# Optimization experiments

Measured on AMD Instinct MI355X. Metric: run time of the kernel, lower is better.

The kernel has to match this reference:

```python
import jax, jax.numpy as jnp
import numpy as np

N = 50000      # nodes
E = 800000     # edges
F = 64         # in_channels == out_channels
ED = 16        # edge_dim
G = 64         # graphs in batch
L = 2          # numLayers
BN_EPS = 1e-5
STD_EPS = 1e-5
AGG_DIM = F * 4 * 3  # 4 aggregators x 3 scalers


def setup_inputs() -> dict:
    key = jax.random.key(0)
    ks = jax.random.split(key, 12)
    r = lambda k, shp, fan: (jax.random.normal(k, shp, jnp.float32) / np.sqrt(fan)).astype(jnp.float32)
    return dict(
        x=jax.random.normal(ks[0], (N, F), jnp.float32),
        edge_attr=jax.random.normal(ks[1], (E, ED), jnp.float32),
        We=r(ks[2], (L, ED, F), ED), be=jnp.zeros((L, F), jnp.float32),
        Wpre=r(ks[3], (L, 3 * F, F), 3 * F), bpre=jnp.zeros((L, F), jnp.float32),
        Wpost=r(ks[4], (L, F + AGG_DIM, F), F + AGG_DIM), bpost=jnp.zeros((L, F), jnp.float32),
        Wlin=r(ks[5], (L, F, F), F), blin=jnp.zeros((L, F), jnp.float32),
        gamma=jnp.ones((L, F), jnp.float32), beta=jnp.zeros((L, F), jnp.float32),
        W1=r(ks[6], (F, 40), F), b1=jnp.zeros((40,), jnp.float32),
        W2=r(ks[7], (40, 1), 40), b2=jnp.zeros((1,), jnp.float32),
        edge_index=jax.random.randint(ks[8], (2, E), 0, N),
        batch=jnp.sort(jax.random.randint(ks[9], (N,), 0, G)),
    )


def _ceal_conv(x, src, dst, edge_attr, We, be, Wpre, bpre, Wpost, bpost, Wlin, blin, deg, amp, att):
    # PNA-style conv, towers=1, pre_layers=post_layers=1
    e = edge_attr @ We + be                                              # [E,F]
    h = jnp.concatenate([x[dst], x[src], e], axis=-1) @ Wpre + bpre      # [E,F]
    degc = jnp.maximum(deg, 1.0)[:, None]
    mean = jax.ops.segment_sum(h, dst, num_segments=N) / degc
    sq = jax.ops.segment_sum(h * h, dst, num_segments=N) / degc
    std = jnp.sqrt(jax.nn.relu(sq - mean * mean) + STD_EPS)
    has = (deg > 0)[:, None]
    mn = jnp.where(has, jax.ops.segment_min(h, dst, num_segments=N), 0.0)
    mx = jnp.where(has, jax.ops.segment_max(h, dst, num_segments=N), 0.0)
    aggs = jnp.concatenate([mean, mn, mx, std], axis=-1)                 # [N,4F]
    scaled = jnp.concatenate([aggs, aggs * amp[:, None], aggs * att[:, None]], axis=-1)  # [N,12F]
    out = jnp.concatenate([x, scaled], axis=-1) @ Wpost + bpost          # [N,F]
    return out @ Wlin + blin


def _bn(x, gamma, beta):
    mu = x.mean(0)
    var = x.var(0)  # biased, as torch BatchNorm training-mode normalization
    return (x - mu) * jax.lax.rsqrt(var + BN_EPS) * gamma + beta


def reference(x, edge_attr, We, be, Wpre, bpre, Wpost, bpost, Wlin, blin,
              gamma, beta, W1, b1, W2, b2, edge_index, batch):
    src, dst = edge_index[0], edge_index[1]
    deg = jax.ops.segment_sum(jnp.ones((E,), jnp.float32), dst, num_segments=N)
    avg_log = jnp.mean(jnp.log(deg + 1.0))
    logd = jnp.log(jnp.maximum(deg, 1.0) + 1.0)
    amp = logd / avg_log
    att = avg_log / logd
    for l in range(L):
        x = _ceal_conv(x, src, dst, edge_attr, We[l], be[l], Wpre[l], bpre[l],
                       Wpost[l], bpost[l], Wlin[l], blin[l], deg, amp, att)
        x = jax.nn.relu(_bn(x, gamma[l], beta[l]))
    cnt = jnp.maximum(jax.ops.segment_sum(jnp.ones((N,), jnp.float32), batch, num_segments=G), 1.0)
    gm = jax.ops.segment_sum(x, batch, num_segments=G) / cnt[:, None]    # global_mean_pool [G,F]
    return jax.nn.relu(gm @ W1 + b1) @ W2 + b2                           # [G,1]
```

## Files before the change

### kernel.cpp

```cpp
#include <hip/hip_runtime.h>
#include <math.h>
#include <float.h>

#define NN 50000
#define EE 800000
#define FF 64
#define EDIM 16
#define GG 64
#define NB64 782
#define NSB 196

typedef short bf16x8 __attribute__((ext_vector_type(8)));
typedef float f32x4 __attribute__((ext_vector_type(4)));

__device__ inline unsigned short bf_rne(float v) {
  unsigned int u = __float_as_uint(v);
  unsigned int r = (u + 0x7FFFu + ((u >> 16) & 1u)) >> 16;
  return (unsigned short)r;
}
__device__ inline float bf_up(unsigned short h) {
  return __uint_as_float(((unsigned int)h) << 16);
}
__device__ inline void split4(float4 v, ushort4& h, ushort4& l) {
  h.x = bf_rne(v.x); h.y = bf_rne(v.y); h.z = bf_rne(v.z); h.w = bf_rne(v.w);
  l.x = bf_rne(v.x - bf_up(h.x));
  l.y = bf_rne(v.y - bf_up(h.y));
  l.z = bf_rne(v.z - bf_up(h.z));
  l.w = bf_rne(v.w - bf_up(h.w));
}

__global__ __launch_bounds__(256) void k_zfill(int* __restrict__ deg, int* __restrict__ cursor,
                                               int* __restrict__ srcs_slack, float* __restrict__ psum) {
  int i = blockIdx.x * 256 + threadIdx.x;
  if (i < NN) { deg[i] = 0; cursor[i] = 0; }
  if (i < 16) srcs_slack[i] = 0;
  if (i < GG * FF + GG) psum[i] = 0.0f;
}

__global__ void k_deg(const int* __restrict__ eidx, int* __restrict__ deg) {
  int e = blockIdx.x * 256 + threadIdx.x;
  if (e < EE) atomicAdd(&deg[eidx[EE + e]], 1);
}

__global__ __launch_bounds__(256) void k_scanA(const int* __restrict__ deg, int* __restrict__ offsets,
                                               int* __restrict__ bsum, float* __restrict__ lsum) {
  __shared__ int ws[4];
  __shared__ float lw[4];
  int t = threadIdx.x;
  int lane = t & 63;
  int wv = t >> 6;
  int i = blockIdx.x * 256 + t;
  int v = (i < NN) ? deg[i] : 0;
  float lg = (i < NN) ? logf((float)v + 1.0f) : 0.0f;
  int x = v;
  #pragma unroll
  for (int o = 1; o < 64; o <<= 1) {
    int y = __shfl_up(x, o);
    if (lane >= o) x += y;
  }
  #pragma unroll
  for (int o = 1; o < 64; o <<= 1) lg += __shfl_xor(lg, o);
  if (lane == 63) ws[wv] = x;
  if (lane == 0) lw[wv] = lg;
  __syncthreads();
  int pre = 0;
  for (int k = 0; k < wv; k++) pre += ws[k];
  if (i < NN) offsets[i] = pre + x - v;
  if (t == 0) {
    bsum[blockIdx.x] = ws[0] + ws[1] + ws[2] + ws[3];
    lsum[blockIdx.x] = lw[0] + lw[1] + lw[2] + lw[3];
  }
}

__global__ __launch_bounds__(256) void k_scanB(const int* __restrict__ bsum, const float* __restrict__ lsum,
                                               int* __restrict__ bpref, float* __restrict__ meta,
                                               float* __restrict__ scbA) {
  __shared__ int ws[4];
  __shared__ float lw[4];
  int t = threadIdx.x;
  int lane = t & 63;
  int wv = t >> 6;
  int v = (t < NSB) ? bsum[t] : 0;
  float lg = (t < NSB) ? lsum[t] : 0.0f;
  int x = v;
  #pragma unroll
  for (int o = 1; o < 64; o <<= 1) {
    int y = __shfl_up(x, o);
    if (lane >= o) x += y;
  }
  #pragma unroll
  for (int o = 1; o < 64; o <<= 1) lg += __shfl_xor(lg, o);
  if (lane == 63) ws[wv] = x;
  if (lane == 0) lw[wv] = lg;
  __syncthreads();
  int pre = 0;
  for (int k = 0; k < wv; k++) pre += ws[k];
  if (t < NSB) bpref[t] = pre + x - v;
  if (t == 0) meta[0] = (lw[0] + lw[1] + lw[2] + lw[3]) / (float)NN;
  if (t < 64) { scbA[t] = 1.0f; scbA[64 + t] = 0.0f; }
  if (t == 0) scbA[128] = -FLT_MAX;
}

__global__ __launch_bounds__(256) void k_scanC(int* __restrict__ offsets, const int* __restrict__ bpref,
                                               const int* __restrict__ deg, const float* __restrict__ meta,
                                               float* __restrict__ amp, float* __restrict__ att) {
  int i = blockIdx.x * 256 + threadIdx.x;
  if (i < NN) {
    offsets[i] += bpref[blockIdx.x];
    float d = (float)deg[i];
    float avg = meta[0];
    float logd = logf(fmaxf(d, 1.0f) + 1.0f);
    amp[i] = logd / avg;
    att[i] = avg / logd;
  }
  if (i == 0) offsets[NN] = EE;
}

__global__ void k_scatter(const int* __restrict__ eidx, const int* __restrict__ offsets,
                          int* __restrict__ cursor, int* __restrict__ srcs,
                          const float* __restrict__ eattr, unsigned int* __restrict__ PermEA) {
  int e = blockIdx.x * 256 + threadIdx.x;
  if (e < EE) {
    int s = eidx[e];
    int d = eidx[EE + e];
    int pos = offsets[d] + atomicAdd(&cursor[d], 1);
    srcs[pos] = s;
    const float4* ep = (const float4*)(eattr + (size_t)e * EDIM);
    float4 q0 = ep[0], q1 = ep[1], q2 = ep[2], q3 = ep[3];
    uint4 pa, pb;
    pa.x = (unsigned)bf_rne(q0.x) | ((unsigned)bf_rne(q0.y) << 16);
    pa.y = (unsigned)bf_rne(q0.z) | ((unsigned)bf_rne(q0.w) << 16);
    pa.z = (unsigned)bf_rne(q1.x) | ((unsigned)bf_rne(q1.y) << 16);
    pa.w = (unsigned)bf_rne(q1.z) | ((unsigned)bf_rne(q1.w) << 16);
    pb.x = (unsigned)bf_rne(q2.x) | ((unsigned)bf_rne(q2.y) << 16);
    pb.y = (unsigned)bf_rne(q2.z) | ((unsigned)bf_rne(q2.w) << 16);
    pb.z = (unsigned)bf_rne(q3.x) | ((unsigned)bf_rne(q3.y) << 16);
    pb.w = (unsigned)bf_rne(q3.z) | ((unsigned)bf_rne(q3.w) << 16);
    ((uint4*)PermEA)[(size_t)pos * 2] = pa;
    ((uint4*)PermEA)[(size_t)pos * 2 + 1] = pb;
  }
}

__global__ __launch_bounds__(256) void k_prep2(const float* __restrict__ We, const float* __restrict__ be,
                                               const float* __restrict__ Wpre, const float* __restrict__ bpre,
                                               const float* __restrict__ Wpost, const float* __restrict__ bpost,
                                               const float* __restrict__ Wlin, const float* __restrict__ blin,
                                               unsigned short* __restrict__ MwT_h, unsigned short* __restrict__ MwT_l,
                                               float* __restrict__ bconst,
                                               unsigned short* __restrict__ WcT_h, unsigned short* __restrict__ WcT_l,
                                               unsigned short* __restrict__ WxT_h, unsigned short* __restrict__ WxT_l,
                                               float* __restrict__ bcomb) {
  int layer = blockIdx.x / 245;
  int blk = blockIdx.x % 245;
  We += (size_t)layer * EDIM * FF;  be += layer * FF;
  Wpre += (size_t)layer * 3 * FF * FF; bpre += layer * FF;
  Wpost += (size_t)layer * 832 * FF; bpost += layer * FF;
  Wlin += (size_t)layer * FF * FF; blin += layer * FF;
  MwT_h += layer * 1024; MwT_l += layer * 1024;
  bconst += layer * FF; bcomb += layer * FF;
  WcT_h += (size_t)layer * 53248; WcT_l += (size_t)layer * 53248;
  WxT_h += layer * 8192; WxT_l += layer * 8192;

  int id = blk * 256 + threadIdx.x;
  if (id < 53248) {
    int k = id >> 6, f = id & 63;
    float a = 0.0f;
    for (int j = 0; j < FF; j++) a += Wpost[(size_t)k * FF + j] * Wlin[j * FF + f];
    unsigned short h = bf_rne(a);
    WcT_h[f * 832 + k] = h;
    WcT_l[f * 832 + k] = bf_rne(a - bf_up(h));
  } else if (id < 61440) {
    int lid = id - 53248;
    int j = lid >> 6, k = lid & 63;
    float v = (j < 64) ? Wpre[k * FF + j] : Wpre[(64 + k) * FF + (j - 64)];
    unsigned short h = bf_rne(v);
    WxT_h[j * 64 + k] = h;
    WxT_l[j * 64 + k] = bf_rne(v - bf_up(h));
  } else if (id < 62464) {
    int lid = id - 61440;
    int k = lid >> 6, f = lid & 63;
    float a = 0.0f;
    for (int j = 0; j < FF; j++) a += We[k * FF + j] * Wpre[(128 + j) * FF + f];
    unsigned short h = bf_rne(a);
    int ct = f & 3, jcol = f >> 2;
    MwT_h[(ct * 16 + jcol) * 16 + k] = h;
    MwT_l[(ct * 16 + jcol) * 16 + k] = bf_rne(a - bf_up(h));
  } else {
    int f = threadIdx.x;
    if (blk == 244 && f < 64) {
      float b = bpre[f];
      for (int j = 0; j < FF; j++) b += be[j] * Wpre[(128 + j) * FF + f];
      bconst[f] = b;
      float c = blin[f];
      for (int j = 0; j < FF; j++) c += bpost[j] * Wlin[j * FF + f];
      bcomb[f] = c;
    }
  }
}

__global__ __launch_bounds__(256) void k_xform(const float* __restrict__ x, const float* __restrict__ scb,
                                               const unsigned short* __restrict__ WxT_h,
                                               const unsigned short* __restrict__ WxT_l,
                                               float* __restrict__ Xd, unsigned short* __restrict__ Xs) {
  __shared__ unsigned short Ah[64 * 72], Al[64 * 72];
  __shared__ unsigned short Bh[128 * 72], Bl[128 * 72];
  int t = threadIdx.x;
  int n0 = blockIdx.x * 64;
  {
    int j = t >> 1, half = t & 1;
    const ushort4* srch = (const ushort4*)(WxT_h + j * 64 + half * 32);
    const ushort4* srcl = (const ushort4*)(WxT_l + j * 64 + half * 32);
    #pragma unroll
    for (int i = 0; i < 8; i++) {
      *(ushort4*)&Bh[j * 72 + half * 32 + i * 4] = srch[i];
      *(ushort4*)&Bl[j * 72 + half * 32 + i * 4] = srcl[i];
    }
  }
  {
    int r = t >> 2, c0 = (t & 3) * 16;
    int n = n0 + r;
    bool rok = n < NN;
    const float4* src = (const float4*)(x + (size_t)n * FF + c0);
    float flr = scb[128];
    #pragma unroll
    for (int c4 = 0; c4 < 4; c4++) {
      float4 v = rok ? src[c4] : make_float4(0.f, 0.f, 0.f, 0.f);
      float4 sc = ((const float4*)scb)[(c0 >> 2) + c4];
      float4 of = ((const float4*)(scb + 64))[(c0 >> 2) + c4];
      v.x = fmaxf(v.x * sc.x + of.x, flr);
      v.y = fmaxf(v.y * sc.y + of.y, flr);
      v.z = fmaxf(v.z * sc.z + of.z, flr);
      v.w = fmaxf(v.w * sc.w + of.w, flr);
      ushort4 h4, l4;
      split4(v, h4, l4);
      *(ushort4*)&Ah[r * 72 + c0 + c4 * 4] = h4;
      *(ushort4*)&Al[r * 72 + c0 + c4 * 4] = l4;
    }
  }
  __syncthreads();
  int lane = t & 63;
  int l15 = lane & 15;
  int quad = lane >> 4;
  int w = __builtin_amdgcn_readfirstlane(t >> 6);
  int rbase = (w & 1) * 32;
  int cbase = (w >> 1) * 64;
  f32x4 acc[2][4];
  #pragma unroll
  for (int rt = 0; rt < 2; rt++)
    #pragma unroll
    for (int ct = 0; ct < 4; ct++) acc[rt][ct] = (f32x4){0.f, 0.f, 0.f, 0.f};

  #pragma unroll
  for (int ks = 0; ks < 2; ks++) {
    bf16x8 a_h[2], a_l[2];
    #pragma unroll
    for (int rt = 0; rt < 2; rt++) {
      int row = rbase + rt * 16 + l15;
      a_h[rt] = *(const bf16x8*)&Ah[row * 72 + ks * 32 + quad * 8];
      a_l[rt] = *(const bf16x8*)&Al[row * 72 + ks * 32 + quad * 8];
    }
    #pragma unroll
    for (int ct = 0; ct < 4; ct++) {
      int col = cbase + ct * 16 + l15;
      bf16x8 b_h = *(const bf16x8*)&Bh[col * 72 + ks * 32 + quad * 8];
      bf16x8 b_l = *(const bf16x8*)&Bl[col * 72 + ks * 32 + quad * 8];
      #pragma unroll
      for (int rt = 0; rt < 2; rt++) {
        acc[rt][ct] = __builtin_amdgcn_mfma_f32_16x16x32_bf16(a_h[rt], b_h, acc[rt][ct], 0, 0, 0);
        acc[rt][ct] = __builtin_amdgcn_mfma_f32_16x16x32_bf16(a_h[rt], b_l, acc[rt][ct], 0, 0, 0);
        acc[rt][ct] = __builtin_amdgcn_mfma_f32_16x16x32_bf16(a_l[rt], b_h, acc[rt][ct], 0, 0, 0);
      }
    }
  }
  #pragma unroll
  for (int rt = 0; rt < 2; rt++) {
    #pragma unroll
    for (int ct = 0; ct < 4; ct++) {
      int col = cbase + ct * 16 + l15;
      #pragma unroll
      for (int reg = 0; reg < 4; reg++) {
        int n = n0 + rbase + rt * 16 + quad * 4 + reg;
        if (n < NN) {
          float v = acc[rt][ct][reg];
          if (col < 64) Xd[(size_t)n * FF + col] = v;
          else          Xs[(size_t)n * FF + (col - 64)] = bf_rne(v);
        }
      }
    }
  }
}

__global__ __launch_bounds__(256) void k_agg(const int* __restrict__ srcs, const int* __restrict__ offsets,
                                             const unsigned int* __restrict__ PermEA,
                                             const unsigned short* __restrict__ MwT_h,
                                             const unsigned short* __restrict__ MwT_l,
                                             const float* __restrict__ bconst,
                                             const float* __restrict__ Xd, const unsigned short* __restrict__ Xs,
                                             unsigned short* __restrict__ aggs) {
  int wid = __builtin_amdgcn_readfirstlane(threadIdx.x >> 6);
  int lane = threadIdx.x & 63;
  int l15 = lane & 15;
  int quad = lane >> 4;
  int n = blockIdx.x * 4 + wid;
  if (n >= NN) return;

  bf16x8 bh[4], bl[4];
  #pragma unroll
  for (int ct = 0; ct < 4; ct++) {
    if (quad < 2) {
      bh[ct] = *(const bf16x8*)&MwT_h[(ct * 16 + l15) * 16 + quad * 8];
      bl[ct] = *(const bf16x8*)&MwT_l[(ct * 16 + l15) * 16 + quad * 8];
    } else {
      bh[ct] = (bf16x8){0, 0, 0, 0, 0, 0, 0, 0};
      bl[ct] = (bf16x8){0, 0, 0, 0, 0, 0, 0, 0};
    }
  }

  float4 xd4 = *(const float4*)(Xd + (size_t)n * FF + 4 * l15);
  float4 bc4 = *(const float4*)(bconst + 4 * l15);
  float bas[4] = {xd4.x + bc4.x, xd4.y + bc4.y, xd4.z + bc4.z, xd4.w + bc4.w};

  int o0 = offsets[n], o1 = offsets[n + 1];
  float s[4]  = {0.f, 0.f, 0.f, 0.f};
  float sq[4] = {0.f, 0.f, 0.f, 0.f};
  float mn[4] = {FLT_MAX, FLT_MAX, FLT_MAX, FLT_MAX};
  float mx[4] = {-FLT_MAX, -FLT_MAX, -FLT_MAX, -FLT_MAX};

  for (int base = o0; base < o1; base += 16) {
    bf16x8 af = (bf16x8){0, 0, 0, 0, 0, 0, 0, 0};
    if (quad < 2) af = *(const bf16x8*)(PermEA + (size_t)(base + l15) * 8 + quad * 4);
    f32x4 acc[4];
    #pragma unroll
    for (int ct = 0; ct < 4; ct++) {
      f32x4 a = (f32x4){0.f, 0.f, 0.f, 0.f};
      a = __builtin_amdgcn_mfma_f32_16x16x32_bf16(af, bl[ct], a, 0, 0, 0);
      a = __builtin_amdgcn_mfma_f32_16x16x32_bf16(af, bh[ct], a, 0, 0, 0);
      acc[ct] = a;
    }
    #pragma unroll
    for (int reg = 0; reg < 4; reg++) {
      int e = base + quad * 4 + reg;
      bool valid = e < o1;
      int ec = min(e, o1 - 1);
      int src = srcs[ec];
      ushort4 xs4 = *(const ushort4*)(Xs + (size_t)src * FF + 4 * l15);
      float xf[4] = {bf_up(xs4.x), bf_up(xs4.y), bf_up(xs4.z), bf_up(xs4.w)};
      #pragma unroll
      for (int ct = 0; ct < 4; ct++) {
        float h = bas[ct] + xf[ct] + acc[ct][reg];
        float hv = valid ? h : 0.0f;
        s[ct] += hv;
        sq[ct] = fmaf(hv, hv, sq[ct]);
        float t1 = fminf(mn[ct], h);
        float t2 = fmaxf(mx[ct], h);
        mn[ct] = valid ? t1 : mn[ct];
        mx[ct] = valid ? t2 : mx[ct];
      }
    }
  }

  #pragma unroll
  for (int ct = 0; ct < 4; ct++) {
    s[ct] += __shfl_xor(s[ct], 16);  s[ct] += __shfl_xor(s[ct], 32);
    sq[ct] += __shfl_xor(sq[ct], 16); sq[ct] += __shfl_xor(sq[ct], 32);
    mn[ct] = fminf(mn[ct], __shfl_xor(mn[ct], 16)); mn[ct] = fminf(mn[ct], __shfl_xor(mn[ct], 32));
    mx[ct] = fmaxf(mx[ct], __shfl_xor(mx[ct], 16)); mx[ct] = fmaxf(mx[ct], __shfl_xor(mx[ct], 32));
  }

  float d = (float)(o1 - o0);
  float dc = fmaxf(d, 1.0f);
  float rdc = 1.0f / dc;
  bool has = d > 0.0f;
  ushort4 outv;
  unsigned short ov[4];
  #pragma unroll
  for (int ct = 0; ct < 4; ct++) {
    float mean = s[ct] * rdc;
    float msq = sq[ct] * rdc;
    float sd = sqrtf(fmaxf(msq - mean * mean, 0.0f) + 1e-5f);
    float vmn = has ? mn[ct] : 0.0f;
    float vmx = has ? mx[ct] : 0.0f;
    float val = (quad == 0) ? mean : (quad == 1) ? vmn : (quad == 2) ? vmx : sd;
    ov[ct] = bf_rne(val);
  }
  outv.x = ov[0]; outv.y = ov[1]; outv.z = ov[2]; outv.w = ov[3];
  *(ushort4*)(aggs + (size_t)n * 256 + quad * 64 + 4 * l15) = outv;
}

__global__ __launch_bounds__(256) void k_post(const float* __restrict__ x, const float* __restrict__ scb,
                                              const unsigned short* __restrict__ aggs,
                                              const float* __restrict__ amp, const float* __restrict__ att,
                                              const unsigned short* __restrict__ WcT_h,
                                              const unsigned short* __restrict__ WcT_l,
                                              const float* __restrict__ bcomb,
                                              float* __restrict__ y, float* __restrict__ partials) {
  __shared__ unsigned short Ah[64 * 72], Al[64 * 72];
  __shared__ unsigned short Bh[64 * 72], Bl[64 * 72];
  __shared__ float red_s[4][32], red_q[4][32];
  int t = threadIdx.x;
  int n0 = blockIdx.x * 64;
  int lane = t & 63;
  int l15 = lane & 15;
  int quad = lane >> 4;
  int w = __builtin_amdgcn_readfirstlane(t >> 6);
  int rbase = (w & 1) * 32;
  int cbase = (w >> 1) * 32;

  int ar = t >> 2;
  int ac0 = (t & 3) * 16;
  int an = n0 + ar;
  bool rok = an < NN;
  const float* xrow = x + (size_t)an * FF;
  const unsigned short* arow = aggs + (size_t)an * 256;
  float flr = scb[128];

  f32x4 acc[3][2][2];
  #pragma unroll
  for (int s = 0; s < 3; s++)
    #pragma unroll
    for (int rt = 0; rt < 2; rt++)
      #pragma unroll
      for (int ct = 0; ct < 2; ct++) acc[s][rt][ct] = (f32x4){0.f, 0.f, 0.f, 0.f};

  {
    #pragma unroll
    for (int c4 = 0; c4 < 4; c4++) {
      float4 v = rok ? *(const float4*)(xrow + ac0 + c4 * 4) : make_float4(0.f, 0.f, 0.f, 0.f);
      float4 sc = ((const float4*)scb)[(ac0 >> 2) + c4];
      float4 of = ((const float4*)(scb + 64))[(ac0 >> 2) + c4];
      v.x = fmaxf(v.x * sc.x + of.x, flr);
      v.y = fmaxf(v.y * sc.y + of.y, flr);
      v.z = fmaxf(v.z * sc.z + of.z, flr);
      v.w = fmaxf(v.w * sc.w + of.w, flr);
      ushort4 h4, l4;
      split4(v, h4, l4);
      *(ushort4*)&Ah[ar * 72 + ac0 + c4 * 4] = h4;
      *(ushort4*)&Al[ar * 72 + ac0 + c4 * 4] = l4;
    }
    const ushort4* sh = (const ushort4*)(WcT_h + ar * 832 + ac0);
    const ushort4* sl = (const ushort4*)(WcT_l + ar * 832 + ac0);
    #pragma unroll
    for (int i = 0; i < 4; i++) {
      *(ushort4*)&Bh[ar * 72 + ac0 + i * 4] = sh[i];
      *(ushort4*)&Bl[ar * 72 + ac0 + i * 4] = sl[i];
    }
    __syncthreads();
    #pragma unroll
    for (int ks = 0; ks < 2; ks++) {
      bf16x8 a_h[2], a_l[2], b_h[2], b_l[2];
      #pragma unroll
      for (int rt = 0; rt < 2; rt++) {
        int row = rbase + rt * 16 + l15;
        a_h[rt] = *(const bf16x8*)&Ah[row * 72 + ks * 32 + quad * 8];
        a_l[rt] = *(const bf16x8*)&Al[row * 72 + ks * 32 + quad * 8];
      }
      #pragma unroll
      for (int ct = 0; ct < 2; ct++) {
        int col = cbase + ct * 16 + l15;
        b_h[ct] = *(const bf16x8*)&Bh[col * 72 + ks * 32 + quad * 8];
        b_l[ct] = *(const bf16x8*)&Bl[col * 72 + ks * 32 + quad * 8];
      }
      #pragma unroll
      for (int rt = 0; rt < 2; rt++)
        #pragma unroll
        for (int ct = 0; ct < 2; ct++) {
          acc[0][rt][ct] = __builtin_amdgcn_mfma_f32_16x16x32_bf16(a_h[rt], b_h[ct], acc[0][rt][ct], 0, 0, 0);
          acc[0][rt][ct] = __builtin_amdgcn_mfma_f32_16x16x32_bf16(a_h[rt], b_l[ct], acc[0][rt][ct], 0, 0, 0);
          acc[0][rt][ct] = __builtin_amdgcn_mfma_f32_16x16x32_bf16(a_l[rt], b_h[ct], acc[0][rt][ct], 0, 0, 0);
        }
    }
    __syncthreads();
  }

  for (int c = 0; c < 4; c++) {
    #pragma unroll
    for (int s = 0; s < 3; s++) {
      if (s == 0) {
        #pragma unroll
        for (int c4 = 0; c4 < 4; c4++) {
          ushort4 u = rok ? *(const ushort4*)(arow + c * 64 + ac0 + c4 * 4) : make_ushort4(0, 0, 0, 0);
          *(ushort4*)&Ah[ar * 72 + ac0 + c4 * 4] = u;
        }
      }
      {
        int kbase = 64 + s * 256 + c * 64;
        const ushort4* sh = (const ushort4*)(WcT_h + ar * 832 + kbase + ac0);
        const ushort4* sl = (const ushort4*)(WcT_l + ar * 832 + kbase + ac0);
        #pragma unroll
        for (int i = 0; i < 4; i++) {
          *(ushort4*)&Bh[ar * 72 + ac0 + i * 4] = sh[i];
          *(ushort4*)&Bl[ar * 72 + ac0 + i * 4] = sl[i];
        }
      }
      __syncthreads();
      #pragma unroll
      for (int ks = 0; ks < 2; ks++) {
        bf16x8 a[2], b_h[2], b_l[2];
        #pragma unroll
        for (int rt = 0; rt < 2; rt++) {
          int row = rbase + rt * 16 + l15;
          a[rt] = *(const bf16x8*)&Ah[row * 72 + ks * 32 + quad * 8];
        }
        #pragma unroll
        for (int ct = 0; ct < 2; ct++) {
          int col = cbase + ct * 16 + l15;
          b_h[ct] = *(const bf16x8*)&Bh[col * 72 + ks * 32 + quad * 8];
          b_l[ct] = *(const bf16x8*)&Bl[col * 72 + ks * 32 + quad * 8];
        }
        #pragma unroll
        for (int rt = 0; rt < 2; rt++)
          #pragma unroll
          for (int ct = 0; ct < 2; ct++) {
            acc[s][rt][ct] = __builtin_amdgcn_mfma_f32_16x16x32_bf16(a[rt], b_h[ct], acc[s][rt][ct], 0, 0, 0);
            acc[s][rt][ct] = __builtin_amdgcn_mfma_f32_16x16x32_bf16(a[rt], b_l[ct], acc[s][rt][ct], 0, 0, 0);
          }
      }
      __syncthreads();
    }
  }

  float ps[2] = {0.f, 0.f}, pq[2] = {0.f, 0.f};
  float bc[2];
  #pragma unroll
  for (int ct = 0; ct < 2; ct++) bc[ct] = bcomb[cbase + ct * 16 + l15];
  #pragma unroll
  for (int rt = 0; rt < 2; rt++) {
    #pragma unroll
    for (int reg = 0; reg < 4; reg++) {
      int n = n0 + rbase + rt * 16 + quad * 4 + reg;
      bool ok = n < NN;
      int nc = min(n, NN - 1);
      float am = amp[nc];
      float at = att[nc];
      #pragma unroll
      for (int ct = 0; ct < 2; ct++) {
        float v = acc[0][rt][ct][reg] + am * acc[1][rt][ct][reg] + at * acc[2][rt][ct][reg] + bc[ct];
        if (ok) {
          y[(size_t)n * FF + (cbase + ct * 16 + l15)] = v;
          ps[ct] += v;
          pq[ct] += v * v;
        }
      }
    }
  }
  #pragma unroll
  for (int ct = 0; ct < 2; ct++) {
    ps[ct] += __shfl_xor(ps[ct], 16);
    ps[ct] += __shfl_xor(ps[ct], 32);
    pq[ct] += __shfl_xor(pq[ct], 16);
    pq[ct] += __shfl_xor(pq[ct], 32);
  }
  if (quad == 0) {
    #pragma unroll
    for (int ct = 0; ct < 2; ct++) {
      red_s[w][ct * 16 + l15] = ps[ct];
      red_q[w][ct * 16 + l15] = pq[ct];
    }
  }
  __syncthreads();
  if (t < 64) {
    float ss, qq;
    if (t < 32) { ss = red_s[0][t] + red_s[1][t]; qq = red_q[0][t] + red_q[1][t]; }
    else        { ss = red_s[2][t - 32] + red_s[3][t - 32]; qq = red_q[2][t - 32] + red_q[3][t - 32]; }
    partials[(size_t)blockIdx.x * 128 + t] = ss;
    partials[(size_t)blockIdx.x * 128 + 64 + t] = qq;
  }
}

__global__ __launch_bounds__(1024) void k_bnfin(const float* __restrict__ partials,
                                                const float* __restrict__ gamma, const float* __restrict__ beta,
                                                float* __restrict__ scb) {
  __shared__ float red[1024];
  __shared__ double tot[128];
  int t = threadIdx.x;
  int c = t & 127, seg = t >> 7;
  float s = 0.f;
  for (int i = seg; i < NB64; i += 8) s += partials[(size_t)i * 128 + c];
  red[t] = s;
  __syncthreads();
  if (t < 128) {
    double d = 0.0;
    #pragma unroll
    for (int sg = 0; sg < 8; sg++) d += (double)red[sg * 128 + t];
    tot[t] = d;
  }
  __syncthreads();
  if (t < 64) {
    double mu = tot[t] / (double)NN;
    double var = tot[64 + t] / (double)NN - mu * mu;
    float sc = gamma[t] * rsqrtf((float)fmax(var, 0.0) + 1e-5f);
    scb[t] = sc;
    scb[64 + t] = beta[t] - (float)mu * sc;
  }
  if (t == 0) scb[128] = 0.0f;
}

__global__ __launch_bounds__(256) void k_pool(const float* __restrict__ x, const float* __restrict__ scb,
                                              const int* __restrict__ batch,
                                              float* __restrict__ psum, float* __restrict__ cnt) {
  int lane = threadIdx.x & 63;
  int wv = threadIdx.x >> 6;
  int wglobal = blockIdx.x * 4 + wv;
  int nw = gridDim.x * 4;
  int per = (NN + nw - 1) / nw;
  int n0 = wglobal * per;
  int n1 = min(n0 + per, NN);
  if (n0 >= n1) return;
  float sc = scb[lane], of = scb[64 + lane], flr = scb[128];
  int gcur = batch[n0];
  float acc = 0.0f;
  int count = 0;
  for (int n = n0; n < n1; n++) {
    int g = batch[n];
    float v = fmaxf(x[(size_t)n * FF + lane] * sc + of, flr);
    if (g != gcur) {
      atomicAdd(&psum[gcur * FF + lane], acc);
      if (lane == 0) atomicAdd(&cnt[gcur], (float)count);
      gcur = g; acc = 0.0f; count = 0;
    }
    acc += v;
    count++;
  }
  atomicAdd(&psum[gcur * FF + lane], acc);
  if (lane == 0) atomicAdd(&cnt[gcur], (float)count);
}

__global__ void k_final(const float* __restrict__ psum, const float* __restrict__ cnt,
                        const float* __restrict__ W1, const float* __restrict__ b1,
                        const float* __restrict__ W2, const float* __restrict__ b2, float* __restrict__ out) {
  int g = threadIdx.x;
  if (g >= GG) return;
  float c = fmaxf(cnt[g], 1.0f);
  float gm[64];
  #pragma unroll
  for (int i = 0; i < 64; i++) gm[i] = psum[g * FF + i] / c;
  float o = b2[0];
  for (int h = 0; h < 40; h++) {
    float a = b1[h];
    #pragma unroll
    for (int i = 0; i < 64; i++) a += gm[i] * W1[i * 40 + h];
    o += fmaxf(a, 0.0f) * W2[h];
  }
  out[g] = o;
}

extern "C" void kernel_launch(void* const* d_in, const int* in_sizes, int n_in,
                              void* d_out, int out_size, void* d_ws, size_t ws_size,
                              hipStream_t stream) {
  (void)in_sizes; (void)n_in; (void)out_size; (void)ws_size;
  const float* x0    = (const float*)d_in[0];
  const float* eattr = (const float*)d_in[1];
  const float* We    = (const float*)d_in[2];
  const float* be    = (const float*)d_in[3];
  const float* Wpre  = (const float*)d_in[4];
  const float* bpre  = (const float*)d_in[5];
  const float* Wpost = (const float*)d_in[6];
  const float* bpost = (const float*)d_in[7];
  const float* Wlin  = (const float*)d_in[8];
  const float* blin  = (const float*)d_in[9];
  const float* gamma = (const float*)d_in[10];
  const float* beta  = (const float*)d_in[11];
  const float* W1    = (const float*)d_in[12];
  const float* b1    = (const float*)d_in[13];
  const float* W2    = (const float*)d_in[14];
  const float* b2    = (const float*)d_in[15];
  const int* eidx    = (const int*)d_in[16];
  const int* batch   = (const int*)d_in[17];
  float* out = (float*)d_out;

  char* w = (char*)d_ws;
  size_t off = 0;
  auto alloc = [&](size_t bytes) -> void* {
    void* p = w + off;
    off += bytes;
    off = (off + 255) & ~(size_t)255;
    return p;
  };
  int*    deg     = (int*)alloc(NN * sizeof(int));
  int*    offsets = (int*)alloc((NN + 1) * sizeof(int));
  int*    cursor  = (int*)alloc(NN * sizeof(int));
  int*    srcs    = (int*)alloc((EE + 16) * sizeof(int));
  unsigned int* PermEA = (unsigned int*)alloc(((size_t)EE + 16) * 8 * sizeof(unsigned int));
  int*    bsum    = (int*)alloc(NSB * sizeof(int));
  int*    bpref   = (int*)alloc(NSB * sizeof(int));
  float*  lsum    = (float*)alloc(NSB * sizeof(float));
  float*  meta    = (float*)alloc(sizeof(float));
  float*  amp     = (float*)alloc(NN * sizeof(float));
  float*  att     = (float*)alloc(NN * sizeof(float));
  unsigned short* MwT_h = (unsigned short*)alloc(2 * FF * EDIM * sizeof(unsigned short));
  unsigned short* MwT_l = (unsigned short*)alloc(2 * FF * EDIM * sizeof(unsigned short));
  float*  bconst  = (float*)alloc(2 * FF * sizeof(float));
  float*  bcomb   = (float*)alloc(2 * FF * sizeof(float));
  float*  scbA    = (float*)alloc(129 * sizeof(float));
  float*  scbB    = (float*)alloc(2 * 129 * sizeof(float));
  unsigned short* WcT_h = (unsigned short*)alloc(2 * (size_t)FF * 832 * sizeof(unsigned short));
  unsigned short* WcT_l = (unsigned short*)alloc(2 * (size_t)FF * 832 * sizeof(unsigned short));
  unsigned short* WxT_h = (unsigned short*)alloc(2 * 128 * 64 * sizeof(unsigned short));
  unsigned short* WxT_l = (unsigned short*)alloc(2 * 128 * 64 * sizeof(unsigned short));
  float*  partials = (float*)alloc((size_t)NB64 * 128 * sizeof(float));
  float*  Xd      = (float*)alloc((size_t)NN * FF * sizeof(float));
  unsigned short* Xs = (unsigned short*)alloc((size_t)NN * FF * sizeof(unsigned short));
  unsigned short* aggs = (unsigned short*)alloc((size_t)NN * 256 * sizeof(unsigned short));
  float*  ybuf    = (float*)alloc((size_t)NN * FF * sizeof(float));
  float*  psum    = (float*)alloc((GG * FF + GG) * sizeof(float));
  float*  cnt     = psum + GG * FF;

  k_zfill<<<NSB, 256, 0, stream>>>(deg, cursor, srcs + EE, psum);
  k_deg<<<(EE + 255) / 256, 256, 0, stream>>>(eidx, deg);
  k_scanA<<<NSB, 256, 0, stream>>>(deg, offsets, bsum, lsum);
  k_scanB<<<1, 256, 0, stream>>>(bsum, lsum, bpref, meta, scbA);
  k_scanC<<<NSB, 256, 0, stream>>>(offsets, bpref, deg, meta, amp, att);
  k_scatter<<<(EE + 255) / 256, 256, 0, stream>>>(eidx, offsets, cursor, srcs, eattr, PermEA);
  k_prep2<<<490, 256, 0, stream>>>(We, be, Wpre, bpre, Wpost, bpost, Wlin, blin,
                                   MwT_h, MwT_l, bconst, WcT_h, WcT_l, WxT_h, WxT_l, bcomb);

  const float* xin = x0;
  const float* scb_in = scbA;
  for (int l = 0; l < 2; l++) {
    k_xform<<<NB64, 256, 0, stream>>>(xin, scb_in, WxT_h + l * 8192, WxT_l + l * 8192, Xd, Xs);
    k_agg<<<(NN + 3) / 4, 256, 0, stream>>>(srcs, offsets, PermEA, MwT_h + l * 1024, MwT_l + l * 1024,
                                            bconst + l * FF, Xd, Xs, aggs);
    k_post<<<NB64, 256, 0, stream>>>(xin, scb_in, aggs, amp, att,
                                     WcT_h + (size_t)l * 53248, WcT_l + (size_t)l * 53248,
                                     bcomb + l * FF, ybuf, partials);
    k_bnfin<<<1, 1024, 0, stream>>>(partials, gamma + l * FF, beta + l * FF, scbB + l * 129);
    xin = ybuf;
    scb_in = scbB + l * 129;
  }
  k_pool<<<200, 256, 0, stream>>>(ybuf, scbB + 129, batch, psum, cnt);
  k_final<<<1, 64, 0, stream>>>(psum, cnt, W1, b1, W2, b2, out);
}
```

Before: 527.2 us.

## Pre-swizzle weights and aggregates into MFMA fragment layout, drop LDS staging

Weight matrices and the aggregated features are now written in a tile layout that matches the MFMA operand fragment, so each lane loads its bf16x8 operand straight from global memory. This removes the LDS staging of B tiles and aggregates, along with most __syncthreads in k_xform and k_post. Each wave now covers all 64 rows and a 16- or 32-column slice, and the BN partial reduction no longer needs shared memory. The trade-off is more redundant global/L2 loads of the weight fragments across waves and blocks, plus a larger padded aggregate buffer.

```diff
diff --git a/kernel.cpp b/kernel.cpp
--- a/kernel.cpp
+++ b/kernel.cpp
@@ -9,6 +9,7 @@
 #define GG 64
 #define NB64 782
 #define NSB 196
+#define NBLK 3128
 
 typedef short bf16x8 __attribute__((ext_vector_type(8)));
 typedef float f32x4 __attribute__((ext_vector_type(4)));
@@ -163,19 +164,30 @@
 
   int id = blk * 256 + threadIdx.x;
   if (id < 53248) {
-    int k = id >> 6, f = id & 63;
+    int kk = id >> 6, f = id & 63;
     float a = 0.0f;
-    for (int j = 0; j < FF; j++) a += Wpost[(size_t)k * FF + j] * Wlin[j * FF + f];
+    for (int j = 0; j < FF; j++) a += Wpost[(size_t)kk * FF + j] * Wlin[j * FF + f];
     unsigned short h = bf_rne(a);
-    WcT_h[f * 832 + k] = h;
-    WcT_l[f * 832 + k] = bf_rne(a - bf_up(h));
+    unsigned short lo = bf_rne(a - bf_up(h));
+    int kc = kk >> 6, krem = kk & 63;
+    int ks = krem >> 5, ksub = krem & 31;
+    int qd = ksub >> 3, el = ksub & 7;
+    int cg = f >> 4, l15 = f & 15;
+    size_t off = (size_t)((cg * 13 + kc) * 2 + ks) * 512 + (qd * 16 + l15) * 8 + el;
+    WcT_h[off] = h;
+    WcT_l[off] = lo;
   } else if (id < 61440) {
     int lid = id - 53248;
     int j = lid >> 6, k = lid & 63;
     float v = (j < 64) ? Wpre[k * FF + j] : Wpre[(64 + k) * FF + (j - 64)];
     unsigned short h = bf_rne(v);
-    WxT_h[j * 64 + k] = h;
-    WxT_l[j * 64 + k] = bf_rne(v - bf_up(h));
+    unsigned short lo = bf_rne(v - bf_up(h));
+    int ks = k >> 5, ksub = k & 31;
+    int qd = ksub >> 3, el = ksub & 7;
+    int cg = j >> 4, l15 = j & 15;
+    int off = ((cg * 2 + ks) * 512) + (qd * 16 + l15) * 8 + el;
+    WxT_h[off] = h;
+    WxT_l[off] = lo;
   } else if (id < 62464) {
     int lid = id - 61440;
     int k = lid >> 6, f = lid & 63;
@@ -203,19 +215,8 @@
                                                const unsigned short* __restrict__ WxT_l,
                                                float* __restrict__ Xd, unsigned short* __restrict__ Xs) {
   __shared__ unsigned short Ah[64 * 72], Al[64 * 72];
-  __shared__ unsigned short Bh[128 * 72], Bl[128 * 72];
   int t = threadIdx.x;
   int n0 = blockIdx.x * 64;
-  {
-    int j = t >> 1, half = t & 1;
-    const ushort4* srch = (const ushort4*)(WxT_h + j * 64 + half * 32);
-    const ushort4* srcl = (const ushort4*)(WxT_l + j * 64 + half * 32);
-    #pragma unroll
-    for (int i = 0; i < 8; i++) {
-      *(ushort4*)&Bh[j * 72 + half * 32 + i * 4] = srch[i];
-      *(ushort4*)&Bl[j * 72 + half * 32 + i * 4] = srcl[i];
-    }
-  }
   {
     int r = t >> 2, c0 = (t & 3) * 16;
     int n = n0 + r;
@@ -242,30 +243,28 @@
   int l15 = lane & 15;
   int quad = lane >> 4;
   int w = __builtin_amdgcn_readfirstlane(t >> 6);
-  int rbase = (w & 1) * 32;
-  int cbase = (w >> 1) * 64;
-  f32x4 acc[2][4];
-  #pragma unroll
-  for (int rt = 0; rt < 2; rt++)
-    #pragma unroll
-    for (int ct = 0; ct < 4; ct++) acc[rt][ct] = (f32x4){0.f, 0.f, 0.f, 0.f};
+  f32x4 acc[4][2];
+  #pragma unroll
+  for (int rt = 0; rt < 4; rt++)
+    #pragma unroll
+    for (int ct = 0; ct < 2; ct++) acc[rt][ct] = (f32x4){0.f, 0.f, 0.f, 0.f};
 
   #pragma unroll
   for (int ks = 0; ks < 2; ks++) {
-    bf16x8 a_h[2], a_l[2];
-    #pragma unroll
-    for (int rt = 0; rt < 2; rt++) {
-      int row = rbase + rt * 16 + l15;
+    bf16x8 a_h[4], a_l[4];
+    #pragma unroll
+    for (int rt = 0; rt < 4; rt++) {
+      int row = rt * 16 + l15;
       a_h[rt] = *(const bf16x8*)&Ah[row * 72 + ks * 32 + quad * 8];
       a_l[rt] = *(const bf16x8*)&Al[row * 72 + ks * 32 + quad * 8];
     }
     #pragma unroll
-    for (int ct = 0; ct < 4; ct++) {
-      int col = cbase + ct * 16 + l15;
-      bf16x8 b_h = *(const bf16x8*)&Bh[col * 72 + ks * 32 + quad * 8];
-      bf16x8 b_l = *(const bf16x8*)&Bl[col * 72 + ks * 32 + quad * 8];
+    for (int ct = 0; ct < 2; ct++) {
+      int T = (w * 2 + ct) * 2 + ks;
+      bf16x8 b_h = *(const bf16x8*)(WxT_h + (size_t)T * 512 + lane * 8);
+      bf16x8 b_l = *(const bf16x8*)(WxT_l + (size_t)T * 512 + lane * 8);
       #pragma unroll
-      for (int rt = 0; rt < 2; rt++) {
+      for (int rt = 0; rt < 4; rt++) {
         acc[rt][ct] = __builtin_amdgcn_mfma_f32_16x16x32_bf16(a_h[rt], b_h, acc[rt][ct], 0, 0, 0);
         acc[rt][ct] = __builtin_amdgcn_mfma_f32_16x16x32_bf16(a_h[rt], b_l, acc[rt][ct], 0, 0, 0);
         acc[rt][ct] = __builtin_amdgcn_mfma_f32_16x16x32_bf16(a_l[rt], b_h, acc[rt][ct], 0, 0, 0);
@@ -273,13 +272,13 @@
     }
   }
   #pragma unroll
-  for (int rt = 0; rt < 2; rt++) {
-    #pragma unroll
-    for (int ct = 0; ct < 4; ct++) {
-      int col = cbase + ct * 16 + l15;
+  for (int rt = 0; rt < 4; rt++) {
+    #pragma unroll
+    for (int ct = 0; ct < 2; ct++) {
+      int col = w * 32 + ct * 16 + l15;
       #pragma unroll
       for (int reg = 0; reg < 4; reg++) {
-        int n = n0 + rbase + rt * 16 + quad * 4 + reg;
+        int n = n0 + rt * 16 + quad * 4 + reg;
         if (n < NN) {
           float v = acc[rt][ct][reg];
           if (col < 64) Xd[(size_t)n * FF + col] = v;
@@ -296,7 +295,7 @@
                                              const unsigned short* __restrict__ MwT_l,
                                              const float* __restrict__ bconst,
                                              const float* __restrict__ Xd, const unsigned short* __restrict__ Xs,
-                                             unsigned short* __restrict__ aggs) {
+                                             unsigned short* __restrict__ aggsF) {
   int wid = __builtin_amdgcn_readfirstlane(threadIdx.x >> 6);
   int lane = threadIdx.x & 63;
   int l15 = lane & 15;
@@ -384,45 +383,39 @@
     ov[ct] = bf_rne(val);
   }
   outv.x = ov[0]; outv.y = ov[1]; outv.z = ov[2]; outv.w = ov[3];
-  *(ushort4*)(aggs + (size_t)n * 256 + quad * 64 + 4 * l15) = outv;
+  {
+    int nblk = n >> 4, r = n & 15;
+    int f0 = 4 * l15;
+    int ksA = f0 >> 5;
+    int qA = (f0 & 31) >> 3;
+    int el = f0 & 7;
+    size_t off = (size_t)((nblk * 4 + quad) * 2 + ksA) * 512 + (qA * 16 + r) * 8 + el;
+    *(ushort4*)(aggsF + off) = outv;
+  }
 }
 
 __global__ __launch_bounds__(256) void k_post(const float* __restrict__ x, const float* __restrict__ scb,
-                                              const unsigned short* __restrict__ aggs,
+                                              const unsigned short* __restrict__ aggsF,
                                               const float* __restrict__ amp, const float* __restrict__ att,
                                               const unsigned short* __restrict__ WcT_h,
                                               const unsigned short* __restrict__ WcT_l,
                                               const float* __restrict__ bcomb,
                                               float* __restrict__ y, float* __restrict__ partials) {
   __shared__ unsigned short Ah[64 * 72], Al[64 * 72];
-  __shared__ unsigned short Bh[64 * 72], Bl[64 * 72];
-  __shared__ float red_s[4][32], red_q[4][32];
   int t = threadIdx.x;
   int n0 = blockIdx.x * 64;
   int lane = t & 63;
   int l15 = lane & 15;
   int quad = lane >> 4;
   int w = __builtin_amdgcn_readfirstlane(t >> 6);
-  int rbase = (w & 1) * 32;
-  int cbase = (w >> 1) * 32;
-
-  int ar = t >> 2;
-  int ac0 = (t & 3) * 16;
-  int an = n0 + ar;
-  bool rok = an < NN;
-  const float* xrow = x + (size_t)an * FF;
-  const unsigned short* arow = aggs + (size_t)an * 256;
-  float flr = scb[128];
-
-  f32x4 acc[3][2][2];
-  #pragma unroll
-  for (int s = 0; s < 3; s++)
-    #pragma unroll
-    for (int rt = 0; rt < 2; rt++)
-      #pragma unroll
-      for (int ct = 0; ct < 2; ct++) acc[s][rt][ct] = (f32x4){0.f, 0.f, 0.f, 0.f};
 
   {
+    int ar = t >> 2;
+    int ac0 = (t & 3) * 16;
+    int an = n0 + ar;
+    bool rok = an < NN;
+    const float* xrow = x + (size_t)an * FF;
+    float flr = scb[128];
     #pragma unroll
     for (int c4 = 0; c4 < 4; c4++) {
       float4 v = rok ? *(const float4*)(xrow + ac0 + c4 * 4) : make_float4(0.f, 0.f, 0.f, 0.f);
@@ -437,133 +430,86 @@
       *(ushort4*)&Ah[ar * 72 + ac0 + c4 * 4] = h4;
       *(ushort4*)&Al[ar * 72 + ac0 + c4 * 4] = l4;
     }
-    const ushort4* sh = (const ushort4*)(WcT_h + ar * 832 + ac0);
-    const ushort4* sl = (const ushort4*)(WcT_l + ar * 832 + ac0);
-    #pragma unroll
-    for (int i = 0; i < 4; i++) {
-      *(ushort4*)&Bh[ar * 72 + ac0 + i * 4] = sh[i];
-      *(ushort4*)&Bl[ar * 72 + ac0 + i * 4] = sl[i];
-    }
-    __syncthreads();
+  }
+  __syncthreads();
+
+  f32x4 acc[3][4];
+  #pragma unroll
+  for (int s = 0; s < 3; s++)
+    #pragma unroll
+    for (int rt = 0; rt < 4; rt++) acc[s][rt] = (f32x4){0.f, 0.f, 0.f, 0.f};
+
+  #pragma unroll
+  for (int ks = 0; ks < 2; ks++) {
+    bf16x8 a_h[4], a_l[4];
+    #pragma unroll
+    for (int rt = 0; rt < 4; rt++) {
+      int row = rt * 16 + l15;
+      a_h[rt] = *(const bf16x8*)&Ah[row * 72 + ks * 32 + quad * 8];
+      a_l[rt] = *(const bf16x8*)&Al[row * 72 + ks * 32 + quad * 8];
+    }
+    int T = (w * 13) * 2 + ks;
+    bf16x8 b_h = *(const bf16x8*)(WcT_h + (size_t)T * 512 + lane * 8);
+    bf16x8 b_l = *(const bf16x8*)(WcT_l + (size_t)T * 512 + lane * 8);
+    #pragma unroll
+    for (int rt = 0; rt < 4; rt++) {
+      acc[0][rt] = __builtin_amdgcn_mfma_f32_16x16x32_bf16(a_h[rt], b_h, acc[0][rt], 0, 0, 0);
+      acc[0][rt] = __builtin_amdgcn_mfma_f32_16x16x32_bf16(a_h[rt], b_l, acc[0][rt], 0, 0, 0);
+      acc[0][rt] = __builtin_amdgcn_mfma_f32_16x16x32_bf16(a_l[rt], b_h, acc[0][rt], 0, 0, 0);
+    }
+  }
+
+  int nb0 = n0 >> 4;
+  #pragma unroll
+  for (int c = 0; c < 4; c++) {
     #pragma unroll
     for (int ks = 0; ks < 2; ks++) {
-      bf16x8 a_h[2], a_l[2], b_h[2], b_l[2];
+      bf16x8 a[4];
       #pragma unroll
-      for (int rt = 0; rt < 2; rt++) {
-        int row = rbase + rt * 16 + l15;
-        a_h[rt] = *(const bf16x8*)&Ah[row * 72 + ks * 32 + quad * 8];
-        a_l[rt] = *(const bf16x8*)&Al[row * 72 + ks * 32 + quad * 8];
+      for (int rt = 0; rt < 4; rt++) {
+        size_t Ta = (size_t)((nb0 + rt) * 4 + c) * 2 + ks;
+        a[rt] = *(const bf16x8*)(aggsF + Ta * 512 + lane * 8);
       }
       #pragma unroll
-      for (int ct = 0; ct < 2; ct++) {
-        int col = cbase + ct * 16 + l15;
-        b_h[ct] = *(const bf16x8*)&Bh[col * 72 + ks * 32 + quad * 8];
-        b_l[ct] = *(const bf16x8*)&Bl[col * 72 + ks * 32 + quad * 8];
-      }
-      #pragma unroll
-      for (int rt = 0; rt < 2; rt++)
+      for (int s = 0; s < 3; s++) {
+        int kc = 1 + s * 4 + c;
+        int T = (w * 13 + kc) * 2 + ks;
+        bf16x8 b_h = *(const bf16x8*)(WcT_h + (size_t)T * 512 + lane * 8);
+        bf16x8 b_l = *(const bf16x8*)(WcT_l + (size_t)T * 512 + lane * 8);
         #pragma unroll
-        for (int ct = 0; ct < 2; ct++) {
-          acc[0][rt][ct] = __builtin_amdgcn_mfma_f32_16x16x32_bf16(a_h[rt], b_h[ct], acc[0][rt][ct], 0, 0, 0);
-          acc[0][rt][ct] = __builtin_amdgcn_mfma_f32_16x16x32_bf16(a_h[rt], b_l[ct], acc[0][rt][ct], 0, 0, 0);
-          acc[0][rt][ct] = __builtin_amdgcn_mfma_f32_16x16x32_bf16(a_l[rt], b_h[ct], acc[0][rt][ct], 0, 0, 0);
-        }
-    }
-    __syncthreads();
-  }
-
-  for (int c = 0; c < 4; c++) {
-    #pragma unroll
-    for (int s = 0; s < 3; s++) {
-      if (s == 0) {
-        #pragma unroll
-        for (int c4 = 0; c4 < 4; c4++) {
-          ushort4 u = rok ? *(const ushort4*)(arow + c * 64 + ac0 + c4 * 4) : make_ushort4(0, 0, 0, 0);
-          *(ushort4*)&Ah[ar * 72 + ac0 + c4 * 4] = u;
+        for (int rt = 0; rt < 4; rt++) {
+          acc[s][rt] = __builtin_amdgcn_mfma_f32_16x16x32_bf16(a[rt], b_h, acc[s][rt], 0, 0, 0);
+          acc[s][rt] = __builtin_amdgcn_mfma_f32_16x16x32_bf16(a[rt], b_l, acc[s][rt], 0, 0, 0);
         }
       }
-      {
-        int kbase = 64 + s * 256 + c * 64;
-        const ushort4* sh = (const ushort4*)(WcT_h + ar * 832 + kbase + ac0);
-        const ushort4* sl = (const ushort4*)(WcT_l + ar * 832 + kbase + ac0);
-        #pragma unroll
-        for (int i = 0; i < 4; i++) {
-          *(ushort4*)&Bh[ar * 72 + ac0 + i * 4] = sh[i];
-          *(ushort4*)&Bl[ar * 72 + ac0 + i * 4] = sl[i];
-        }
-      }
-      __syncthreads();
-      #pragma unroll
-      for (int ks = 0; ks < 2; ks++) {
-        bf16x8 a[2], b_h[2], b_l[2];
-        #pragma unroll
-        for (int rt = 0; rt < 2; rt++) {
-          int row = rbase + rt * 16 + l15;
-          a[rt] = *(const bf16x8*)&Ah[row * 72 + ks * 32 + quad * 8];
-        }
-        #pragma unroll
-        for (int ct = 0; ct < 2; ct++) {
-          int col = cbase + ct * 16 + l15;
-          b_h[ct] = *(const bf16x8*)&Bh[col * 72 + ks * 32 + quad * 8];
-          b_l[ct] = *(const bf16x8*)&Bl[col * 72 + ks * 32 + quad * 8];
-        }
-        #pragma unroll
-        for (int rt = 0; rt < 2; rt++)
-          #pragma unroll
-          for (int ct = 0; ct < 2; ct++) {
-            acc[s][rt][ct] = __builtin_amdgcn_mfma_f32_16x16x32_bf16(a[rt], b_h[ct], acc[s][rt][ct], 0, 0, 0);
-            acc[s][rt][ct] = __builtin_amdgcn_mfma_f32_16x16x32_bf16(a[rt], b_l[ct], acc[s][rt][ct], 0, 0, 0);
-          }
-      }
-      __syncthreads();
-    }
-  }
-
-  float ps[2] = {0.f, 0.f}, pq[2] = {0.f, 0.f};
-  float bc[2];
-  #pragma unroll
-  for (int ct = 0; ct < 2; ct++) bc[ct] = bcomb[cbase + ct * 16 + l15];
-  #pragma unroll
-  for (int rt = 0; rt < 2; rt++) {
+    }
+  }
+
+  int col = w * 16 + l15;
+  float bc = bcomb[col];
+  float ps = 0.f, pq = 0.f;
+  #pragma unroll
+  for (int rt = 0; rt < 4; rt++) {
     #pragma unroll
     for (int reg = 0; reg < 4; reg++) {
-      int n = n0 + rbase + rt * 16 + quad * 4 + reg;
+      int n = n0 + rt * 16 + quad * 4 + reg;
       bool ok = n < NN;
       int nc = min(n, NN - 1);
       float am = amp[nc];
       float at = att[nc];
-      #pragma unroll
-      for (int ct = 0; ct < 2; ct++) {
-        float v = acc[0][rt][ct][reg] + am * acc[1][rt][ct][reg] + at * acc[2][rt][ct][reg] + bc[ct];
-        if (ok) {
-          y[(size_t)n * FF + (cbase + ct * 16 + l15)] = v;
-          ps[ct] += v;
-          pq[ct] += v * v;
-        }
+      float v = acc[0][rt][reg] + am * acc[1][rt][reg] + at * acc[2][rt][reg] + bc;
+      if (ok) {
+        y[(size_t)n * FF + col] = v;
+        ps += v;
+        pq += v * v;
       }
     }
   }
-  #pragma unroll
-  for (int ct = 0; ct < 2; ct++) {
-    ps[ct] += __shfl_xor(ps[ct], 16);
-    ps[ct] += __shfl_xor(ps[ct], 32);
-    pq[ct] += __shfl_xor(pq[ct], 16);
-    pq[ct] += __shfl_xor(pq[ct], 32);
-  }
+  ps += __shfl_xor(ps, 16); ps += __shfl_xor(ps, 32);
+  pq += __shfl_xor(pq, 16); pq += __shfl_xor(pq, 32);
   if (quad == 0) {
-    #pragma unroll
-    for (int ct = 0; ct < 2; ct++) {
-      red_s[w][ct * 16 + l15] = ps[ct];
-      red_q[w][ct * 16 + l15] = pq[ct];
-    }
-  }
-  __syncthreads();
-  if (t < 64) {
-    float ss, qq;
-    if (t < 32) { ss = red_s[0][t] + red_s[1][t]; qq = red_q[0][t] + red_q[1][t]; }
-    else        { ss = red_s[2][t - 32] + red_s[3][t - 32]; qq = red_q[2][t - 32] + red_q[3][t - 32]; }
-    partials[(size_t)blockIdx.x * 128 + t] = ss;
-    partials[(size_t)blockIdx.x * 128 + 64 + t] = qq;
+    partials[(size_t)blockIdx.x * 128 + col] = ps;
+    partials[(size_t)blockIdx.x * 128 + 64 + col] = pq;
   }
 }
 
@@ -700,7 +646,7 @@
   float*  partials = (float*)alloc((size_t)NB64 * 128 * sizeof(float));
   float*  Xd      = (float*)alloc((size_t)NN * FF * sizeof(float));
   unsigned short* Xs = (unsigned short*)alloc((size_t)NN * FF * sizeof(unsigned short));
-  unsigned short* aggs = (unsigned short*)alloc((size_t)NN * 256 * sizeof(unsigned short));
+  unsigned short* aggsF = (unsigned short*)alloc((size_t)NBLK * 4096 * sizeof(unsigned short));
   float*  ybuf    = (float*)alloc((size_t)NN * FF * sizeof(float));
   float*  psum    = (float*)alloc((GG * FF + GG) * sizeof(float));
   float*  cnt     = psum + GG * FF;
@@ -719,8 +665,8 @@
   for (int l = 0; l < 2; l++) {
     k_xform<<<NB64, 256, 0, stream>>>(xin, scb_in, WxT_h + l * 8192, WxT_l + l * 8192, Xd, Xs);
     k_agg<<<(NN + 3) / 4, 256, 0, stream>>>(srcs, offsets, PermEA, MwT_h + l * 1024, MwT_l + l * 1024,
-                                            bconst + l * FF, Xd, Xs, aggs);
-    k_post<<<NB64, 256, 0, stream>>>(xin, scb_in, aggs, amp, att,
+                                            bconst + l * FF, Xd, Xs, aggsF);
+    k_post<<<NB64, 256, 0, stream>>>(xin, scb_in, aggsF, amp, att,
                                      WcT_h + (size_t)l * 53248, WcT_l + (size_t)l * 53248,
                                      bcomb + l * FF, ybuf, partials);
     k_bnfin<<<1, 1024, 0, stream>>>(partials, gamma + l * FF, beta + l * FF, scbB + l * 129);
```

After: 530.3 us. Within noise of the previous version (+0.6%).
